# Optimization experiments

Measured on AMD Instinct MI355X. Metric: run time of the kernel, lower is better.

## Reference

```python
import jax, jax.numpy as jnp
import numpy as np
from jax import lax

B, N, S, H = 8, 32, 512, 768   # batch, max spans, seq len, bert hidden
K, C, L = 3, 128, 64           # conv kernel height, cnn_hidden_size, num labels


def setup_inputs() -> dict:
    key = jax.random.key(0)
    ks = jax.random.split(key, 9)
    rng = np.random.default_rng(0)
    W = 16  # max span width
    starts = rng.integers(0, S - W, size=(B, N))
    widths = rng.integers(1, W + 1, size=(B, N))
    starts[0, 0], widths[0, 0] = 100, W        # force max span width = 16
    starts[0, 1], widths[0, 1] = S - W, 1      # force max prefix width = 496
    starts[0, 2], widths[0, 2] = 0, 1          # force min end = 1 -> max suffix = 511
    ends = starts + widths
    spans_dranges = jnp.asarray(np.stack([starts, ends], axis=-1), dtype=jnp.int32)
    sc = 0.02
    return {
        "tokens_emb": jax.random.normal(ks[0], (B, S, H), jnp.float32),
        "span_w": jax.random.normal(ks[1], (C, H, K), jnp.float32) * sc,
        "span_b": jax.random.normal(ks[2], (C,), jnp.float32) * sc,
        "prefix_w": jax.random.normal(ks[3], (C, H, K), jnp.float32) * sc,
        "prefix_b": jax.random.normal(ks[4], (C,), jnp.float32) * sc,
        "suffix_w": jax.random.normal(ks[5], (C, H, K), jnp.float32) * sc,
        "suffix_b": jax.random.normal(ks[6], (C,), jnp.float32) * sc,
        "fc_w": jax.random.normal(ks[7], (L, 3 * C), jnp.float32) * sc,
        "fc_b": jax.random.normal(ks[8], (L,), jnp.float32) * sc,
        "spans_dranges": spans_dranges,
        "word_seq_lengths": jnp.full((B,), S, dtype=jnp.int32),
        "max_span_width": W,
        "max_prefix_width": S - W,
        "max_suffix_width": S - 1,
    }


def _conv_pool(x, w, b):
    # x: [BN, T, H]; Conv2d(H->C, kernel (K,1)) over time + max_pool over all valid positions
    T = x.shape[1]
    if T < K:  # original pads with zeros up to kernel size
        x = jnp.pad(x, ((0, 0), (0, K - T), (0, 0)))
    y = lax.conv_general_dilated(x.transpose(0, 2, 1), w, (1,), 'VALID',
                                 dimension_numbers=('NCH', 'OIH', 'NCH'))  # [BN, C, T-K+1]
    return (y + b[None, :, None]).max(axis=2)  # pool_filter_size == full output length


def reference(tokens_emb, span_w, span_b, prefix_w, prefix_b, suffix_w, suffix_b,
              fc_w, fc_b, spans_dranges, word_seq_lengths,
              max_span_width, max_prefix_width, max_suffix_width):
    starts = spans_dranges[..., 0]  # [B,N]
    ends = spans_dranges[..., 1]

    def gather(idx, mask):
        # idx, mask: [B,N,W] -> zero-padded per-span token embeddings [B*N, W, H]
        g = jnp.take_along_axis(tokens_emb[:, None], jnp.clip(idx, 0, S - 1)[..., None], axis=2)
        return (g * mask[..., None]).reshape(B * N, -1, H)

    ar = jnp.arange(max_span_width)
    span_x = gather(starts[..., None] + ar, ar < (ends - starts)[..., None])
    arp = jnp.arange(max_prefix_width)
    prefix_x = gather(jnp.broadcast_to(arp, (B, N, max_prefix_width)), arp < starts[..., None])
    ars = jnp.arange(max_suffix_width)
    suffix_x = gather(ends[..., None] + ars,
                      ars < (word_seq_lengths[:, None, None] - ends[..., None]))

    feats = jnp.concatenate([
        _conv_pool(prefix_x, prefix_w, prefix_b),
        _conv_pool(span_x, span_w, span_b),
        _conv_pool(suffix_x, suffix_w, suffix_b),
    ], axis=-1)  # [B*N, 3C]
    probs = jax.nn.sigmoid(feats @ fc_w.T + fc_b)  # [B*N, L]
    pred_ids = (probs > 0.5).astype(jnp.int32).reshape(B, N, L)
    return probs, pred_ids
```

## Files before the change

### kernel.cpp

```cpp
#include <hip/hip_runtime.h>
#include <hip/hip_bf16.h>
#include <math.h>

#define NEG_INF (-1e30f)

typedef _Float16 half8 __attribute__((ext_vector_type(8)));
typedef _Float16 half4 __attribute__((ext_vector_type(4)));
typedef float f32x4 __attribute__((ext_vector_type(4)));
typedef float f32x16 __attribute__((ext_vector_type(16)));

__device__ __forceinline__ void load_lds16(const void* g, void* l) {
  __builtin_amdgcn_global_load_lds((const __attribute__((address_space(1))) void*)g,
                                   (__attribute__((address_space(3))) void*)l, 16, 0, 0);
}

__global__ __launch_bounds__(256) void prep(
    const float* __restrict__ tokens, const float* __restrict__ span_w,
    const float* __restrict__ prefix_w, const float* __restrict__ suffix_w,
    const float* __restrict__ fc_w, _Float16* __restrict__ A2,
    _Float16* __restrict__ Bt, float* __restrict__ fcT) {
  int bid = blockIdx.x;
  int t = threadIdx.x;
  if (bid < 3072) {
    int g4 = (bid * 256 + t) * 4;
    int m = g4 / 768, h = g4 % 768;
    float4 x = *(const float4*)(tokens + g4);
    float xs[4] = {x.x, x.y, x.z, x.w};
    half4 hi, lo;
#pragma unroll
    for (int i = 0; i < 4; ++i) {
      _Float16 h_ = (_Float16)xs[i];
      hi[i] = h_;
      lo[i] = (_Float16)((xs[i] - (float)h_) * 64.0f);
    }
    size_t base = (size_t)m * 1536 + h;
    *(half4*)(A2 + base) = hi;
    *(half4*)(A2 + base + 768) = lo;
  } else if (bid < 3216) {
    int g = (bid - 3072) * 256 + t;
    int ws = g / 12288;
    int r = g % 12288;
    int c = r / 96, h = (r % 96) * 8;
    const float* wsrc = (ws == 0) ? prefix_w : (ws == 1) ? span_w : suffix_w;
    const float* src = wsrc + (size_t)(c * 768 + h) * 3;
    float wv[24];
#pragma unroll
    for (int i = 0; i < 6; ++i) *(float4*)&wv[i * 4] = *(const float4*)(src + i * 4);
#pragma unroll
    for (int tap = 0; tap < 3; ++tap) {
      half8 hi, lo;
#pragma unroll
      for (int i = 0; i < 8; ++i) {
        float x = wv[i * 3 + tap];
        _Float16 h_ = (_Float16)x;
        hi[i] = h_;
        lo[i] = (_Float16)((x - (float)h_) * 64.0f);
      }
      size_t jb = (size_t)(ws * 384 + tap * 128 + c) * 1536 + h;
      *(half8*)(Bt + jb) = hi;
      *(half8*)(Bt + jb + 768) = lo;
    }
  } else {
    int g = (bid - 3216) * 256 + t;
    int i = g >> 6, c = g & 63;
    fcT[g] = fc_w[c * 384 + i];
  }
}

__global__ __launch_bounds__(256) void gemm_f16(const _Float16* __restrict__ A2,
                                                const _Float16* __restrict__ Bt,
                                                float* __restrict__ Ct) {
  __shared__ _Float16 As[2][128 * 64];
  __shared__ _Float16 Bs[2][128 * 64];
  const int bm = blockIdx.x * 128;
  const int bj = blockIdx.y * 128;
  const int tid = threadIdx.x;
  const int w = tid >> 6;
  const int lane = tid & 63;
  const int srow = tid >> 3;
  const int phys = tid & 7;
  const int clog = phys ^ (srow & 7);
  const int srcoff = (clog >> 2) * 768 + (clog & 3) * 8;
  const _Float16* gA = A2 + (size_t)(bm + srow) * 1536 + srcoff;
  const _Float16* gB = Bt + (size_t)(bj + srow) * 1536 + srcoff;
  const size_t rstep = (size_t)32 * 1536;
  const int l31 = lane & 31;
  const int hi32 = lane >> 5;
  const int sw = lane & 7;
  const int m0w = (w & 1) * 64;
  const int n0w = (w >> 1) * 64;
#define CO(p, ks) ((((p) * 4 + (ks) * 2 + hi32) ^ sw) * 8)
  f32x16 aa[2][2], ab[2][2];
#pragma unroll
  for (int i = 0; i < 2; ++i)
#pragma unroll
    for (int j = 0; j < 2; ++j)
#pragma unroll
      for (int q = 0; q < 16; ++q) {
        aa[i][j][q] = 0.f;
        ab[i][j][q] = 0.f;
      }

#pragma unroll
  for (int p = 0; p < 4; ++p) {
    load_lds16(gA + (size_t)p * rstep, &As[0][p * 2048 + w * 512]);
    load_lds16(gB + (size_t)p * rstep, &Bs[0][p * 2048 + w * 512]);
  }

  for (int i = 0; i < 24; ++i) {
    const int cur = i & 1;
    __syncthreads();
    if (i + 1 < 24) {
      const int kp = (i + 1) * 32;
      const int nxt = cur ^ 1;
#pragma unroll
      for (int p = 0; p < 4; ++p) {
        load_lds16(gA + kp + (size_t)p * rstep, &As[nxt][p * 2048 + w * 512]);
        load_lds16(gB + kp + (size_t)p * rstep, &Bs[nxt][p * 2048 + w * 512]);
      }
    }
#pragma unroll
    for (int ks = 0; ks < 2; ++ks) {
      half8 a0[2], a1[2], b0[2], b1[2];
#pragma unroll
      for (int mp = 0; mp < 2; ++mp) {
        const int row = (m0w + mp * 32 + l31) * 64;
        a0[mp] = *(const half8*)&As[cur][row + CO(0, ks)];
        a1[mp] = *(const half8*)&As[cur][row + CO(1, ks)];
      }
#pragma unroll
      for (int np = 0; np < 2; ++np) {
        const int row = (n0w + np * 32 + l31) * 64;
        b0[np] = *(const half8*)&Bs[cur][row + CO(0, ks)];
        b1[np] = *(const half8*)&Bs[cur][row + CO(1, ks)];
      }
#pragma unroll
      for (int mp = 0; mp < 2; ++mp)
#pragma unroll
        for (int np = 0; np < 2; ++np) {
          aa[mp][np] = __builtin_amdgcn_mfma_f32_32x32x16_f16(a0[mp], b0[np], aa[mp][np], 0, 0, 0);
          ab[mp][np] = __builtin_amdgcn_mfma_f32_32x32x16_f16(a1[mp], b0[np], ab[mp][np], 0, 0, 0);
          ab[mp][np] = __builtin_amdgcn_mfma_f32_32x32x16_f16(a0[mp], b1[np], ab[mp][np], 0, 0, 0);
        }
    }
  }
#undef CO
#pragma unroll
  for (int mp = 0; mp < 2; ++mp)
#pragma unroll
    for (int np = 0; np < 2; ++np) {
      const int n_out = bj + n0w + np * 32 + l31;
      float* cp = Ct + (size_t)n_out * 4096 + bm + m0w + mp * 32 + 4 * hi32;
#pragma unroll
      for (int r = 0; r < 4; ++r) {
        f32x4 v;
#pragma unroll
        for (int q = 0; q < 4; ++q)
          v[q] = aa[mp][np][4 * r + q] + 0.015625f * ab[mp][np][4 * r + q];
        *(f32x4*)(cp + 8 * r) = v;
      }
    }
}

__global__ __launch_bounds__(256) void scan_kernel(const float* __restrict__ Ct,
                                                   const int* __restrict__ wsl,
                                                   float* __restrict__ PM2,
                                                   float* __restrict__ SM2) {
  int pair = blockIdx.x * 4 + (threadIdx.x >> 6);
  int b = pair >> 7;
  int c = pair & 127;
  int lane = threadIdx.x & 63;
  int mb = b * 512;
  int t0 = lane * 8;
  const float* p0 = Ct + (size_t)(0 + c) * 4096 + mb;
  const float* p1 = Ct + (size_t)(128 + c) * 4096 + mb;
  const float* p2 = Ct + (size_t)(256 + c) * 4096 + mb;
  float v[8];
#pragma unroll
  for (int i = 0; i < 8; i++) {
    int t = t0 + i;
    v[i] = (t < 494) ? (p0[t] + p1[t + 1] + p2[t + 2]) : NEG_INF;
  }
#pragma unroll
  for (int i = 1; i < 8; i++) v[i] = fmaxf(v[i], v[i - 1]);
  float x = v[7];
#pragma unroll
  for (int d = 1; d < 64; d <<= 1) {
    float y = __shfl_up(x, d);
    if (lane >= d) x = fmaxf(x, y);
  }
  float excl = __shfl_up(x, 1);
  if (lane == 0) excl = NEG_INF;
  float* pm = PM2 + (size_t)pair * 512;
#pragma unroll
  for (int i = 0; i < 8; i++) {
    int t = t0 + i;
    if (t < 494) pm[t] = fmaxf(v[i], excl);
  }
  const float* s0 = Ct + (size_t)(768 + c) * 4096 + mb;
  const float* s1 = Ct + (size_t)(896 + c) * 4096 + mb;
  const float* s2 = Ct + (size_t)(1024 + c) * 4096 + mb;
  int qmax = wsl[b] - 3;
  if (qmax > 509) qmax = 509;
  float u[8];
#pragma unroll
  for (int i = 0; i < 8; i++) {
    int q = t0 + i;
    u[i] = (q <= qmax) ? (s0[q] + s1[q + 1] + s2[q + 2]) : NEG_INF;
  }
#pragma unroll
  for (int i = 6; i >= 0; i--) u[i] = fmaxf(u[i], u[i + 1]);
  float xr = u[0];
#pragma unroll
  for (int d = 1; d < 64; d <<= 1) {
    float y = __shfl_down(xr, d);
    if (lane < 64 - d) xr = fmaxf(xr, y);
  }
  float exclr = __shfl_down(xr, 1);
  if (lane == 63) exclr = NEG_INF;
  float* sm = SM2 + (size_t)pair * 512;
#pragma unroll
  for (int i = 0; i < 8; i++) sm[t0 + i] = fmaxf(u[i], exclr);
}

__global__ __launch_bounds__(128) void span_kernel(
    const float* __restrict__ Ct, const float* __restrict__ PM2,
    const float* __restrict__ SM2, const float* __restrict__ prefix_b,
    const float* __restrict__ span_b, const float* __restrict__ suffix_b,
    const float* __restrict__ fcT, const float* __restrict__ fc_b,
    const int* __restrict__ spans, const int* __restrict__ wsl,
    float* __restrict__ out) {
  __shared__ float sfeat[384];
  __shared__ float part[64];
  int sp = blockIdx.x;
  int b = sp >> 5;
  int c = threadIdx.x;
  int s = spans[sp * 2], e = spans[sp * 2 + 1];
  int Lb = wsl[b];
  int mb = b * 512;
  {
    const float* t0p = Ct + (size_t)c * 4096 + mb;
    const float* t1p = Ct + (size_t)(128 + c) * 4096 + mb;
    float m = NEG_INF;
    if (s >= 3) m = fmaxf(m, PM2[(size_t)(b * 128 + c) * 512 + s - 3]);
    if (s >= 2 && s <= 495) m = fmaxf(m, t0p[s - 2] + t1p[s - 1]);
    if (s >= 1 && s <= 494) m = fmaxf(m, t0p[s - 1]);
    if (s <= 493) m = fmaxf(m, 0.0f);
    sfeat[c] = m + prefix_b[c];
  }
  {
    const float* u0 = Ct + (size_t)(384 + c) * 4096 + mb;
    const float* u1 = Ct + (size_t)(512 + c) * 4096 + mb;
    const float* u2 = Ct + (size_t)(640 + c) * 4096 + mb;
    int w = e - s;
    float m = NEG_INF;
    for (int p = 0; p + 2 < w; ++p)
      m = fmaxf(m, u0[s + p] + u1[s + p + 1] + u2[s + p + 2]);
    if (w >= 2 && w <= 15) m = fmaxf(m, u0[s + w - 2] + u1[s + w - 1]);
    if (w <= 14) m = fmaxf(m, u0[s + w - 1]);
    if (w <= 13) m = fmaxf(m, 0.0f);
    sfeat[128 + c] = m + span_b[c];
  }
  {
    const float* x0 = Ct + (size_t)(768 + c) * 4096 + mb;
    const float* x1 = Ct + (size_t)(896 + c) * 4096 + mb;
    float m = NEG_INF;
    if (e <= Lb - 3) m = fmaxf(m, SM2[(size_t)(b * 128 + c) * 512 + e]);
    if (Lb - 2 - e >= 0 && Lb - 2 - e <= 508)
      m = fmaxf(m, x0[Lb - 2] + x1[Lb - 1]);
    if (Lb - 1 - e >= 0 && Lb - 1 - e <= 508) m = fmaxf(m, x0[Lb - 1]);
    if (Lb - e <= 508) m = fmaxf(m, 0.0f);
    sfeat[256 + c] = m + suffix_b[c];
  }
  __syncthreads();
  {
    int cc = threadIdx.x & 63;
    int half = threadIdx.x >> 6;
    float acc2 = 0.0f;
    const float* fp = fcT + (size_t)(half * 192) * 64 + cc;
    const float* sf = sfeat + half * 192;
#pragma unroll 8
    for (int i = 0; i < 192; ++i) acc2 = fmaf(sf[i], fp[(size_t)i * 64], acc2);
    if (half) part[cc] = acc2;
    __syncthreads();
    if (!half) {
      float a = acc2 + part[cc] + fc_b[cc];
      float pr = 1.0f / (1.0f + expf(-a));
      out[sp * 64 + cc] = pr;
      out[16384 + sp * 64 + cc] = (pr > 0.5f) ? 1.0f : 0.0f;
    }
  }
}

extern "C" void kernel_launch(void* const* d_in, const int* in_sizes, int n_in,
                              void* d_out, int out_size, void* d_ws,
                              size_t ws_size, hipStream_t stream) {
  const float* tokens = (const float*)d_in[0];
  const float* span_w = (const float*)d_in[1];
  const float* span_b = (const float*)d_in[2];
  const float* prefix_w = (const float*)d_in[3];
  const float* prefix_b = (const float*)d_in[4];
  const float* suffix_w = (const float*)d_in[5];
  const float* suffix_b = (const float*)d_in[6];
  const float* fc_w = (const float*)d_in[7];
  const float* fc_b = (const float*)d_in[8];
  const int* spans = (const int*)d_in[9];
  const int* wsl = (const int*)d_in[10];
  float* out = (float*)d_out;

  char* ws = (char*)d_ws;
  float* Ct = (float*)ws;
  _Float16* A2 = (_Float16*)(ws + 18874368);
  _Float16* Bt = (_Float16*)(ws + 31457280);
  float* PM2 = (float*)(ws + 34996224);
  float* SM2 = (float*)(ws + 37093376);
  float* fcT = (float*)(ws + 39190528);

  hipLaunchKernelGGL(prep, dim3(3312), dim3(256), 0, stream, tokens, span_w,
                     prefix_w, suffix_w, fc_w, A2, Bt, fcT);
  hipLaunchKernelGGL(gemm_f16, dim3(32, 9), dim3(256), 0, stream, A2, Bt, Ct);
  hipLaunchKernelGGL(scan_kernel, dim3(256), dim3(256), 0, stream, Ct, wsl,
                     PM2, SM2);
  hipLaunchKernelGGL(span_kernel, dim3(256), dim3(128), 0, stream, Ct, PM2,
                     SM2, prefix_b, span_b, suffix_b, fcT, fc_b, spans, wsl,
                     out);
}
```

Measured before the change: 152.0 us.

## Split GEMM K dimension across two blocks and sum partials in consumers

Splits the fp16 hi/lo GEMM reduction over H into two halves along a new grid z dimension, doubling the block count from 288 to 576 to fill more compute units. Each half writes its own partial Ct buffer, and the scan and span kernels add the two partials on every read. In exchange, the Ct write and read traffic and the workspace size double.

```diff
diff --git a/kernel.cpp b/kernel.cpp
--- a/kernel.cpp
+++ b/kernel.cpp
@@ -3,6 +3,8 @@
 #include <math.h>
 
 #define NEG_INF (-1e30f)
+#define CT_HALF 4718592
+#define CS(P, i) ((P)[i] + (P)[CT_HALF + (i)])
 
 typedef _Float16 half8 __attribute__((ext_vector_type(8)));
 typedef _Float16 half4 __attribute__((ext_vector_type(4)));
@@ -74,6 +76,7 @@
   __shared__ _Float16 Bs[2][128 * 64];
   const int bm = blockIdx.x * 128;
   const int bj = blockIdx.y * 128;
+  const int kz = blockIdx.z;
   const int tid = threadIdx.x;
   const int w = tid >> 6;
   const int lane = tid & 63;
@@ -81,8 +84,8 @@
   const int phys = tid & 7;
   const int clog = phys ^ (srow & 7);
   const int srcoff = (clog >> 2) * 768 + (clog & 3) * 8;
-  const _Float16* gA = A2 + (size_t)(bm + srow) * 1536 + srcoff;
-  const _Float16* gB = Bt + (size_t)(bj + srow) * 1536 + srcoff;
+  const _Float16* gA = A2 + (size_t)(bm + srow) * 1536 + kz * 384 + srcoff;
+  const _Float16* gB = Bt + (size_t)(bj + srow) * 1536 + kz * 384 + srcoff;
   const size_t rstep = (size_t)32 * 1536;
   const int l31 = lane & 31;
   const int hi32 = lane >> 5;
@@ -107,10 +110,10 @@
     load_lds16(gB + (size_t)p * rstep, &Bs[0][p * 2048 + w * 512]);
   }
 
-  for (int i = 0; i < 24; ++i) {
+  for (int i = 0; i < 12; ++i) {
     const int cur = i & 1;
     __syncthreads();
-    if (i + 1 < 24) {
+    if (i + 1 < 12) {
       const int kp = (i + 1) * 32;
       const int nxt = cur ^ 1;
 #pragma unroll
@@ -145,12 +148,13 @@
     }
   }
 #undef CO
+  float* outC = Ct + (size_t)kz * CT_HALF;
 #pragma unroll
   for (int mp = 0; mp < 2; ++mp)
 #pragma unroll
     for (int np = 0; np < 2; ++np) {
       const int n_out = bj + n0w + np * 32 + l31;
-      float* cp = Ct + (size_t)n_out * 4096 + bm + m0w + mp * 32 + 4 * hi32;
+      float* cp = outC + (size_t)n_out * 4096 + bm + m0w + mp * 32 + 4 * hi32;
 #pragma unroll
       for (int r = 0; r < 4; ++r) {
         f32x4 v;
@@ -179,7 +183,7 @@
 #pragma unroll
   for (int i = 0; i < 8; i++) {
     int t = t0 + i;
-    v[i] = (t < 494) ? (p0[t] + p1[t + 1] + p2[t + 2]) : NEG_INF;
+    v[i] = (t < 494) ? (CS(p0, t) + CS(p1, t + 1) + CS(p2, t + 2)) : NEG_INF;
   }
 #pragma unroll
   for (int i = 1; i < 8; i++) v[i] = fmaxf(v[i], v[i - 1]);
@@ -206,7 +210,7 @@
 #pragma unroll
   for (int i = 0; i < 8; i++) {
     int q = t0 + i;
-    u[i] = (q <= qmax) ? (s0[q] + s1[q + 1] + s2[q + 2]) : NEG_INF;
+    u[i] = (q <= qmax) ? (CS(s0, q) + CS(s1, q + 1) + CS(s2, q + 2)) : NEG_INF;
   }
 #pragma unroll
   for (int i = 6; i >= 0; i--) u[i] = fmaxf(u[i], u[i + 1]);
@@ -243,8 +247,8 @@
     const float* t1p = Ct + (size_t)(128 + c) * 4096 + mb;
     float m = NEG_INF;
     if (s >= 3) m = fmaxf(m, PM2[(size_t)(b * 128 + c) * 512 + s - 3]);
-    if (s >= 2 && s <= 495) m = fmaxf(m, t0p[s - 2] + t1p[s - 1]);
-    if (s >= 1 && s <= 494) m = fmaxf(m, t0p[s - 1]);
+    if (s >= 2 && s <= 495) m = fmaxf(m, CS(t0p, s - 2) + CS(t1p, s - 1));
+    if (s >= 1 && s <= 494) m = fmaxf(m, CS(t0p, s - 1));
     if (s <= 493) m = fmaxf(m, 0.0f);
     sfeat[c] = m + prefix_b[c];
   }
@@ -255,9 +259,9 @@
     int w = e - s;
     float m = NEG_INF;
     for (int p = 0; p + 2 < w; ++p)
-      m = fmaxf(m, u0[s + p] + u1[s + p + 1] + u2[s + p + 2]);
-    if (w >= 2 && w <= 15) m = fmaxf(m, u0[s + w - 2] + u1[s + w - 1]);
-    if (w <= 14) m = fmaxf(m, u0[s + w - 1]);
+      m = fmaxf(m, CS(u0, s + p) + CS(u1, s + p + 1) + CS(u2, s + p + 2));
+    if (w >= 2 && w <= 15) m = fmaxf(m, CS(u0, s + w - 2) + CS(u1, s + w - 1));
+    if (w <= 14) m = fmaxf(m, CS(u0, s + w - 1));
     if (w <= 13) m = fmaxf(m, 0.0f);
     sfeat[128 + c] = m + span_b[c];
   }
@@ -267,8 +271,8 @@
     float m = NEG_INF;
     if (e <= Lb - 3) m = fmaxf(m, SM2[(size_t)(b * 128 + c) * 512 + e]);
     if (Lb - 2 - e >= 0 && Lb - 2 - e <= 508)
-      m = fmaxf(m, x0[Lb - 2] + x1[Lb - 1]);
-    if (Lb - 1 - e >= 0 && Lb - 1 - e <= 508) m = fmaxf(m, x0[Lb - 1]);
+      m = fmaxf(m, CS(x0, Lb - 2) + CS(x1, Lb - 1));
+    if (Lb - 1 - e >= 0 && Lb - 1 - e <= 508) m = fmaxf(m, CS(x0, Lb - 1));
     if (Lb - e <= 508) m = fmaxf(m, 0.0f);
     sfeat[256 + c] = m + suffix_b[c];
   }
@@ -310,15 +314,15 @@
 
   char* ws = (char*)d_ws;
   float* Ct = (float*)ws;
-  _Float16* A2 = (_Float16*)(ws + 18874368);
-  _Float16* Bt = (_Float16*)(ws + 31457280);
-  float* PM2 = (float*)(ws + 34996224);
-  float* SM2 = (float*)(ws + 37093376);
-  float* fcT = (float*)(ws + 39190528);
+  _Float16* A2 = (_Float16*)(ws + 37748736);
+  _Float16* Bt = (_Float16*)(ws + 50331648);
+  float* PM2 = (float*)(ws + 53870592);
+  float* SM2 = (float*)(ws + 55967744);
+  float* fcT = (float*)(ws + 58064896);
 
   hipLaunchKernelGGL(prep, dim3(3312), dim3(256), 0, stream, tokens, span_w,
                      prefix_w, suffix_w, fc_w, A2, Bt, fcT);
-  hipLaunchKernelGGL(gemm_f16, dim3(32, 9), dim3(256), 0, stream, A2, Bt, Ct);
+  hipLaunchKernelGGL(gemm_f16, dim3(32, 9, 2), dim3(256), 0, stream, A2, Bt, Ct);
   hipLaunchKernelGGL(scan_kernel, dim3(256), dim3(256), 0, stream, Ct, wsl,
                      PM2, SM2);
   hipLaunchKernelGGL(span_kernel, dim3(256), dim3(128), 0, stream, Ct, PM2,
```

Result: slower. 158.6 us (+4.4%).
